# Kernel tuning notes

Hardware: AMD Instinct MI355X
Metric: run time of the kernel (lower is better)

The kernel has to match this reference:

```python
import jax, jax.numpy as jnp
import numpy as np

B, N, D = 128, 512, 128      # graphs, nodes/graph, feature dim
KEEP_RATIO = 0.5
K = int(KEEP_RATIO * N)      # kept nodes per graph (fixed -> jit friendly)
EDGE_P = 0.05                # random graph edge density


def setup_inputs() -> dict:
    key = jax.random.key(0)
    k1, k2, k3 = jax.random.split(key, 3)
    # random symmetric binary adjacency without self loops, per graph block
    u = jax.random.uniform(k1, (B, N, N))
    a0 = (u < EDGE_P).astype(jnp.float32)
    a0 = jnp.maximum(a0, jnp.swapaxes(a0, 1, 2))
    eye = jnp.eye(N, dtype=jnp.float32)
    a0 = a0 * (1.0 - eye)
    # normalized input adjacency: D^-0.5 (A0 + I) D^-0.5 (as `normalization` does)
    a_hat = a0 + eye
    dinv = a_hat.sum(-1) ** -0.5
    adjacency = a_hat * dinv[:, :, None] * dinv[:, None, :]   # [B,N,N]
    input_feature = jax.random.normal(k2, (B, N, D), dtype=jnp.float32)
    graph_indicator = jnp.repeat(jnp.arange(B, dtype=jnp.int32), N)  # [B*N]
    # attn_gcn params: Linear(D -> 1) kaiming-style init, zero bias
    weight = jax.random.normal(k3, (D, 1), dtype=jnp.float32) * (2.0 / D) ** 0.5
    bias = jnp.zeros((1,), dtype=jnp.float32)
    return {"adjacency": adjacency, "input_feature": input_feature,
            "graph_indicator": graph_indicator, "weight": weight, "bias": bias}


def reference(adjacency, input_feature, graph_indicator, weight, bias):
    # --- attention GCN: Z = A @ (X W) + b, then tanh ---
    support = jnp.einsum('bnd,do->bno', input_feature, weight)      # [B,N,1]
    score = jnp.einsum('bnm,bmo->bno', adjacency, support) + bias   # [B,N,1]
    attn = jnp.tanh(score[..., 0])                                  # [B,N]
    # --- top_rank: per-graph top-K by score; mask preserves node order ---
    _, idx = jax.lax.top_k(attn, K)                                 # [B,K]
    idx = jnp.sort(idx, axis=-1)                                    # original node order
    # --- hidden = X[mask] * attn[mask] ---
    kept_x = jnp.take_along_axis(input_feature, idx[:, :, None], axis=1)  # [B,K,D]
    kept_s = jnp.take_along_axis(attn, idx, axis=1)                       # [B,K]
    hidden = (kept_x * kept_s[:, :, None]).reshape(B * K, D)
    mask_graph_indicator = jnp.repeat(jnp.arange(B, dtype=graph_indicator.dtype), K)
    # --- filter_adjacency: binarize off-diagonal structure, gather, renormalize ---
    eye_n = jnp.eye(N, dtype=adjacency.dtype)
    a_bin = jnp.where((adjacency != 0) & (eye_n == 0), 1.0, 0.0)    # [B,N,N]
    rows = jnp.take_along_axis(a_bin, idx[:, :, None], axis=1)      # [B,K,N]
    sub = jnp.take_along_axis(rows, idx[:, None, :], axis=2)        # [B,K,K]
    a_hat = sub + jnp.eye(K, dtype=adjacency.dtype)
    dinv = a_hat.sum(-1) ** -0.5
    mask_adjacency = a_hat * dinv[:, :, None] * dinv[:, None, :]    # [B,K,K]
    return hidden, mask_graph_indicator, mask_adjacency
```

## Files before the change

kernel.cpp:

```cpp
#include <hip/hip_runtime.h>
#include <hip/hip_bf16.h>
#include <math.h>

#define BGR 128
#define NND 512
#define DFD 128
#define KKP 256

typedef unsigned int uint;
typedef unsigned long long ull;

__global__ __launch_bounds__(256) void k_support(const float* __restrict__ X,
                                                 const float* __restrict__ W,
                                                 float* __restrict__ sup) {
    __shared__ float w_s[DFD];
    int t = threadIdx.x;
    if (t < DFD) w_s[t] = W[t];
    __syncthreads();
    int node = blockIdx.x * 64 + (t >> 2);
    int q = t & 3;
    const float4* xp = (const float4*)(X + (size_t)node * DFD + q * 32);
    const float4* wp = (const float4*)(w_s + q * 32);
    float sum = 0.f;
#pragma unroll
    for (int i = 0; i < 8; ++i) {
        float4 x = xp[i], w = wp[i];
        sum += x.x * w.x + x.y * w.y + x.z * w.z + x.w * w.w;
    }
    sum += __shfl_xor(sum, 1);
    sum += __shfl_xor(sum, 2);
    if (q == 0) sup[node] = sum;
}

__global__ __launch_bounds__(256) void k_score(const float* __restrict__ A,
                                               const float* __restrict__ sup,
                                               const float* __restrict__ bias,
                                               float* __restrict__ attn,
                                               ull* __restrict__ bm) {
    __shared__ float sup_s[NND];
    int b = blockIdx.x >> 6;
    int rblk = blockIdx.x & 63;
    int t = threadIdx.x;
    sup_s[t] = sup[b * NND + t];
    sup_s[256 + t] = sup[b * NND + 256 + t];
    __syncthreads();
    int wave = t >> 6, l = t & 63;
    float bias0 = bias[0];
    const float4* sp = (const float4*)sup_s;
    float4 s0 = sp[l], s1 = sp[64 + l];
#pragma unroll
    for (int r = 0; r < 2; ++r) {
        int row = rblk * 8 + wave * 2 + r;
        const float4* ap = (const float4*)(A + ((size_t)b * NND + row) * NND);
        float4 a0 = ap[l], a1 = ap[64 + l];
        float sum = a0.x * s0.x + a0.y * s0.y + a0.z * s0.z + a0.w * s0.w
                  + a1.x * s1.x + a1.y * s1.y + a1.z * s1.z + a1.w * s1.w;
        int c0 = 4 * l;
        ull m[8];
        m[0] = __ballot(a0.x != 0.f && (c0 + 0) != row);
        m[1] = __ballot(a0.y != 0.f && (c0 + 1) != row);
        m[2] = __ballot(a0.z != 0.f && (c0 + 2) != row);
        m[3] = __ballot(a0.w != 0.f && (c0 + 3) != row);
        m[4] = __ballot(a1.x != 0.f && (256 + c0 + 0) != row);
        m[5] = __ballot(a1.y != 0.f && (256 + c0 + 1) != row);
        m[6] = __ballot(a1.z != 0.f && (256 + c0 + 2) != row);
        m[7] = __ballot(a1.w != 0.f && (256 + c0 + 3) != row);
#pragma unroll
        for (int off = 32; off >= 1; off >>= 1) sum += __shfl_down(sum, off);
        if (l == 0) {
            attn[b * NND + row] = tanhf(sum + bias0);
            ull* bp = bm + ((size_t)b * NND + row) * 8;
#pragma unroll
            for (int k = 0; k < 8; ++k) bp[k] = m[k];
        }
    }
}

__global__ __launch_bounds__(512) void k_fuse(const float* __restrict__ X,
                                              const float* __restrict__ attn,
                                              const uint* __restrict__ bm,
                                              float* __restrict__ out_hidden,
                                              float* __restrict__ out_gi,
                                              uint* __restrict__ bits,
                                              float* __restrict__ dinv) {
    __shared__ float attn_s[NND];
    __shared__ uint km[16];
    __shared__ int idx_s[KKP];
    __shared__ uint4 bm_s4[KKP][4];
    __shared__ uint bits_s[KKP][8];
    int b = blockIdx.x, t = threadIdx.x;
    attn_s[t] = attn[b * NND + t];
    __syncthreads();
    int wave = t >> 6, l = t & 63;

    float a = attn_s[t];
    int r = 0;
    const float4* ap4 = (const float4*)attn_s;
    for (int jj = 0; jj < 128; ++jj) {
        float4 v = ap4[jj];
        int j0 = jj * 4;
        r += (v.x > a || (v.x == a && j0     < t)) ? 1 : 0;
        r += (v.y > a || (v.y == a && j0 + 1 < t)) ? 1 : 0;
        r += (v.z > a || (v.z == a && j0 + 2 < t)) ? 1 : 0;
        r += (v.w > a || (v.w == a && j0 + 3 < t)) ? 1 : 0;
    }
    bool keep = r < KKP;
    ull mk = __ballot(keep);
    if (l == 0) { km[wave * 2] = (uint)mk; km[wave * 2 + 1] = (uint)(mk >> 32); }
    __syncthreads();
    if (keep) {
        int w = t >> 5, pos = 0;
        for (int u = 0; u < w; ++u) pos += __popc(km[u]);
        pos += __popc(km[w] & ((1u << (t & 31)) - 1u));
        idx_s[pos] = t;
    }
    if (t < KKP) out_gi[b * KKP + t] = (float)b;
    __syncthreads();

    {
        int i = t >> 1, half = t & 1;
        const uint4* src = (const uint4*)(bm + ((size_t)b * NND + idx_s[i]) * 16) + half * 2;
        bm_s4[i][half * 2]     = src[0];
        bm_s4[i][half * 2 + 1] = src[1];
    }
    __syncthreads();

    const uint* bmw = (const uint*)bm_s4;
    int j = t & 255;
    int jn = idx_s[j];
    int widx = ((jn >> 8) * 4 + (jn & 3)) * 2 + ((jn >> 7) & 1);
    int bitpos = (jn >> 2) & 31;
    int rowoff = t >> 8;
    int wq = (t >> 6) & 3;
    for (int ii = 0; ii < KKP; ii += 2) {
        int row = ii + rowoff;
        uint kb = (bmw[row * 16 + widx] >> bitpos) & 1u;
        ull mb = __ballot(kb != 0u);
        if (l == 0) {
            bits_s[row][wq * 2]     = (uint)mb;
            bits_s[row][wq * 2 + 1] = (uint)(mb >> 32);
            uint* gp = bits + ((size_t)b * KKP + row) * 8 + wq * 2;
            gp[0] = (uint)mb;
            gp[1] = (uint)(mb >> 32);
        }
    }
    __syncthreads();
    if (t < KKP) {
        int s = 1;
#pragma unroll
        for (int k = 0; k < 8; ++k) s += __popc(bits_s[t][k]);
        dinv[b * KKP + t] = 1.0f / sqrtf((float)s);
    }

    for (int r2 = 0; r2 < 32; ++r2) {
        int k = wave * 32 + r2;
        int node = idx_s[k];
        float s = attn_s[node];
        const float2* xp = (const float2*)(X + ((size_t)b * NND + node) * DFD);
        float2 v = xp[l];
        v.x *= s; v.y *= s;
        ((float2*)(out_hidden + ((size_t)b * KKP + k) * DFD))[l] = v;
    }
}

__global__ __launch_bounds__(256) void k_norm(const uint* __restrict__ bits,
                                              const float* __restrict__ dinv,
                                              float* __restrict__ out_adj) {
    __shared__ float dinv_s[KKP];
    int b = blockIdx.x >> 5;
    int rblk = blockIdx.x & 31;
    int t = threadIdx.x, wave = t >> 6, l = t & 63;
    dinv_s[t] = dinv[b * KKP + t];
    __syncthreads();
    float4 dj = ((const float4*)dinv_s)[l];
    const float* djp = &dj.x;
#pragma unroll
    for (int r = 0; r < 2; ++r) {
        int i = rblk * 8 + wave * 2 + r;
        float di = dinv_s[i];
        const uint* bp = bits + ((size_t)b * KKP + i) * 8;
        uint word = bp[l >> 3];
        int j0 = l * 4;
        float4 v;
        float* pv = &v.x;
#pragma unroll
        for (int c = 0; c < 4; ++c) {
            int j = j0 + c;
            float ah = ((word >> (j & 31)) & 1u) ? 1.0f : 0.0f;
            if (j == i) ah += 1.0f;
            pv[c] = ah * di * djp[c];
        }
        ((float4*)(out_adj + ((size_t)b * KKP + i) * KKP))[l] = v;
    }
}

extern "C" void kernel_launch(void* const* d_in, const int* in_sizes, int n_in,
                              void* d_out, int out_size, void* d_ws, size_t ws_size,
                              hipStream_t stream) {
    const float* A    = (const float*)d_in[0];
    const float* X    = (const float*)d_in[1];
    const float* W    = (const float*)d_in[3];
    const float* bias = (const float*)d_in[4];

    float* out        = (float*)d_out;
    float* out_hidden = out;
    float* out_gi     = out + (size_t)BGR * KKP * DFD;
    float* out_adj    = out_gi + (size_t)BGR * KKP;

    float* sup  = (float*)d_ws;
    float* attn = sup + (size_t)BGR * NND;
    ull*   bm   = (ull*)(attn + (size_t)BGR * NND);
    uint*  bits = (uint*)(bm + (size_t)BGR * NND * 8);
    float* dinv = (float*)(bits + (size_t)BGR * KKP * 8);

    k_support<<<BGR * NND / 64, 256, 0, stream>>>(X, W, sup);
    k_score<<<BGR * 64, 256, 0, stream>>>(A, sup, bias, attn, bm);
    k_fuse<<<BGR, 512, 0, stream>>>(X, attn, (const uint*)bm, out_hidden, out_gi, bits, dinv);
    k_norm<<<BGR * 32, 256, 0, stream>>>(bits, dinv, out_adj);
}
```

Baseline: 71.01 us.

## Move hidden-feature gather out of per-graph kernel into wide tail kernel

The gather-and-scale of kept node features was done by only 128 blocks inside the per-graph selection kernel. It now runs in a new tail kernel with thousands of blocks, which also takes over the adjacency normalization work in fewer, larger blocks. The selection kernel writes the kept indices to a workspace buffer. The goal is to spread the 16MB hidden copy across the whole GPU instead of 128 blocks, at the cost of an extra global index write and read.

```diff
diff --git a/kernel.cpp b/kernel.cpp
--- a/kernel.cpp
+++ b/kernel.cpp
@@ -6,6 +6,7 @@
 #define NND 512
 #define DFD 128
 #define KKP 256
+#define HIDBLK 4096
 
 typedef unsigned int uint;
 typedef unsigned long long ull;
@@ -76,11 +77,10 @@
     }
 }
 
-__global__ __launch_bounds__(512) void k_fuse(const float* __restrict__ X,
-                                              const float* __restrict__ attn,
+__global__ __launch_bounds__(512) void k_fuse(const float* __restrict__ attn,
                                               const uint* __restrict__ bm,
-                                              float* __restrict__ out_hidden,
                                               float* __restrict__ out_gi,
+                                              int* __restrict__ gidx,
                                               uint* __restrict__ bits,
                                               float* __restrict__ dinv) {
     __shared__ float attn_s[NND];
@@ -113,6 +113,7 @@
         for (int u = 0; u < w; ++u) pos += __popc(km[u]);
         pos += __popc(km[w] & ((1u << (t & 31)) - 1u));
         idx_s[pos] = t;
+        gidx[b * KKP + pos] = t;
     }
     if (t < KKP) out_gi[b * KKP + t] = (float)b;
     __syncthreads();
@@ -151,46 +152,55 @@
         for (int k = 0; k < 8; ++k) s += __popc(bits_s[t][k]);
         dinv[b * KKP + t] = 1.0f / sqrtf((float)s);
     }
-
-    for (int r2 = 0; r2 < 32; ++r2) {
-        int k = wave * 32 + r2;
-        int node = idx_s[k];
-        float s = attn_s[node];
-        const float2* xp = (const float2*)(X + ((size_t)b * NND + node) * DFD);
-        float2 v = xp[l];
-        v.x *= s; v.y *= s;
-        ((float2*)(out_hidden + ((size_t)b * KKP + k) * DFD))[l] = v;
-    }
-}
-
-__global__ __launch_bounds__(256) void k_norm(const uint* __restrict__ bits,
+}
+
+__global__ __launch_bounds__(256) void k_tail(const float* __restrict__ X,
+                                              const float* __restrict__ attn,
+                                              const int* __restrict__ gidx,
+                                              const uint* __restrict__ bits,
                                               const float* __restrict__ dinv,
+                                              float* __restrict__ out_hidden,
                                               float* __restrict__ out_adj) {
     __shared__ float dinv_s[KKP];
-    int b = blockIdx.x >> 5;
-    int rblk = blockIdx.x & 31;
+    int blk = blockIdx.x;
     int t = threadIdx.x, wave = t >> 6, l = t & 63;
-    dinv_s[t] = dinv[b * KKP + t];
-    __syncthreads();
-    float4 dj = ((const float4*)dinv_s)[l];
-    const float* djp = &dj.x;
-#pragma unroll
-    for (int r = 0; r < 2; ++r) {
-        int i = rblk * 8 + wave * 2 + r;
-        float di = dinv_s[i];
-        const uint* bp = bits + ((size_t)b * KKP + i) * 8;
-        uint word = bp[l >> 3];
-        int j0 = l * 4;
-        float4 v;
-        float* pv = &v.x;
-#pragma unroll
-        for (int c = 0; c < 4; ++c) {
-            int j = j0 + c;
-            float ah = ((word >> (j & 31)) & 1u) ? 1.0f : 0.0f;
-            if (j == i) ah += 1.0f;
-            pv[c] = ah * di * djp[c];
-        }
-        ((float4*)(out_adj + ((size_t)b * KKP + i) * KKP))[l] = v;
+    if (blk < HIDBLK) {
+        int r0 = blk * 8 + wave * 2;
+#pragma unroll
+        for (int rr = 0; rr < 2; ++rr) {
+            int r = r0 + rr;
+            int b = r >> 8;
+            int node = gidx[r];
+            float s = attn[b * NND + node];
+            const float2* xp = (const float2*)(X + ((size_t)b * NND + node) * DFD);
+            float2 v = xp[l];
+            v.x *= s; v.y *= s;
+            ((float2*)(out_hidden + (size_t)r * DFD))[l] = v;
+        }
+    } else {
+        int nb = blk - HIDBLK;
+        int b = nb >> 2, q = nb & 3;
+        if (t < KKP) dinv_s[t] = dinv[b * KKP + t];
+        __syncthreads();
+        float4 dj = ((const float4*)dinv_s)[l];
+        const float* djp = &dj.x;
+        for (int rr = 0; rr < 16; ++rr) {
+            int i = q * 64 + wave * 16 + rr;
+            float di = dinv_s[i];
+            const uint* bp = bits + ((size_t)b * KKP + i) * 8;
+            uint word = bp[l >> 3];
+            int j0 = l * 4;
+            float4 v;
+            float* pv = &v.x;
+#pragma unroll
+            for (int c = 0; c < 4; ++c) {
+                int j = j0 + c;
+                float ah = ((word >> (j & 31)) & 1u) ? 1.0f : 0.0f;
+                if (j == i) ah += 1.0f;
+                pv[c] = ah * di * djp[c];
+            }
+            ((float4*)(out_adj + ((size_t)b * KKP + i) * KKP))[l] = v;
+        }
     }
 }
 
@@ -212,9 +222,11 @@
     ull*   bm   = (ull*)(attn + (size_t)BGR * NND);
     uint*  bits = (uint*)(bm + (size_t)BGR * NND * 8);
     float* dinv = (float*)(bits + (size_t)BGR * KKP * 8);
+    int*   gidx = (int*)(dinv + (size_t)BGR * KKP);
 
     k_support<<<BGR * NND / 64, 256, 0, stream>>>(X, W, sup);
     k_score<<<BGR * 64, 256, 0, stream>>>(A, sup, bias, attn, bm);
-    k_fuse<<<BGR, 512, 0, stream>>>(X, attn, (const uint*)bm, out_hidden, out_gi, bits, dinv);
-    k_norm<<<BGR * 32, 256, 0, stream>>>(bits, dinv, out_adj);
-}
+    k_fuse<<<BGR, 512, 0, stream>>>(attn, (const uint*)bm, out_gi, gidx, bits, dinv);
+    k_tail<<<HIDBLK + BGR * 4, 256, 0, stream>>>(X, attn, gidx, bits, dinv,
+                                                 out_hidden, out_adj);
+}
```

Measured after the change: 70.53 us. About the same (-0.7%).

## Fuse top-k selection and adjacency normalization into one per-graph-quarter kernel

Applied to the files above, without the earlier changes.

Merges the selection kernel and the normalized-adjacency kernel into a single kernel launched with four blocks per graph. Each block recomputes the ranking and the sub-adjacency bitmask in shared memory, then writes only its quarter of the hidden rows and adjacency rows. This removes one launch and the global-memory round trip for the intermediate bits and dinv buffers, and spreads the work over four times as many blocks. In exchange, the rank computation and bitmask extraction are done four times per graph.

```diff
diff --git a/kernel.cpp b/kernel.cpp
--- a/kernel.cpp
+++ b/kernel.cpp
@@ -76,22 +76,22 @@
     }
 }
 
-__global__ __launch_bounds__(512) void k_fuse(const float* __restrict__ X,
+__global__ __launch_bounds__(512) void k_mega(const float* __restrict__ X,
                                               const float* __restrict__ attn,
                                               const uint* __restrict__ bm,
                                               float* __restrict__ out_hidden,
                                               float* __restrict__ out_gi,
-                                              uint* __restrict__ bits,
-                                              float* __restrict__ dinv) {
+                                              float* __restrict__ out_adj) {
     __shared__ float attn_s[NND];
     __shared__ uint km[16];
     __shared__ int idx_s[KKP];
     __shared__ uint4 bm_s4[KKP][4];
     __shared__ uint bits_s[KKP][8];
-    int b = blockIdx.x, t = threadIdx.x;
+    __shared__ float dinv_s[KKP];
+    int b = blockIdx.x >> 2, q = blockIdx.x & 3;
+    int t = threadIdx.x, wave = t >> 6, l = t & 63;
     attn_s[t] = attn[b * NND + t];
     __syncthreads();
-    int wave = t >> 6, l = t & 63;
 
     float a = attn_s[t];
     int r = 0;
@@ -114,7 +114,6 @@
         pos += __popc(km[w] & ((1u << (t & 31)) - 1u));
         idx_s[pos] = t;
     }
-    if (t < KKP) out_gi[b * KKP + t] = (float)b;
     __syncthreads();
 
     {
@@ -123,11 +122,22 @@
         bm_s4[i][half * 2]     = src[0];
         bm_s4[i][half * 2 + 1] = src[1];
     }
+
+    if (t < KKP) out_gi[b * KKP + t] = (float)b;
+#pragma unroll
+    for (int it = 0; it < 8; ++it) {
+        int k = q * 64 + it * 8 + wave;
+        int node = idx_s[k];
+        float s = attn_s[node];
+        const float2* xp = (const float2*)(X + ((size_t)b * NND + node) * DFD);
+        float2 v = xp[l];
+        v.x *= s; v.y *= s;
+        ((float2*)(out_hidden + ((size_t)b * KKP + k) * DFD))[l] = v;
+    }
     __syncthreads();
 
     const uint* bmw = (const uint*)bm_s4;
-    int j = t & 255;
-    int jn = idx_s[j];
+    int jn = idx_s[t & 255];
     int widx = ((jn >> 8) * 4 + (jn & 3)) * 2 + ((jn >> 7) & 1);
     int bitpos = (jn >> 2) & 31;
     int rowoff = t >> 8;
@@ -139,9 +149,6 @@
         if (l == 0) {
             bits_s[row][wq * 2]     = (uint)mb;
             bits_s[row][wq * 2 + 1] = (uint)(mb >> 32);
-            uint* gp = bits + ((size_t)b * KKP + row) * 8 + wq * 2;
-            gp[0] = (uint)mb;
-            gp[1] = (uint)(mb >> 32);
         }
     }
     __syncthreads();
@@ -149,37 +156,17 @@
         int s = 1;
 #pragma unroll
         for (int k = 0; k < 8; ++k) s += __popc(bits_s[t][k]);
-        dinv[b * KKP + t] = 1.0f / sqrtf((float)s);
-    }
-
-    for (int r2 = 0; r2 < 32; ++r2) {
-        int k = wave * 32 + r2;
-        int node = idx_s[k];
-        float s = attn_s[node];
-        const float2* xp = (const float2*)(X + ((size_t)b * NND + node) * DFD);
-        float2 v = xp[l];
-        v.x *= s; v.y *= s;
-        ((float2*)(out_hidden + ((size_t)b * KKP + k) * DFD))[l] = v;
-    }
-}
-
-__global__ __launch_bounds__(256) void k_norm(const uint* __restrict__ bits,
-                                              const float* __restrict__ dinv,
-                                              float* __restrict__ out_adj) {
-    __shared__ float dinv_s[KKP];
-    int b = blockIdx.x >> 5;
-    int rblk = blockIdx.x & 31;
-    int t = threadIdx.x, wave = t >> 6, l = t & 63;
-    dinv_s[t] = dinv[b * KKP + t];
-    __syncthreads();
+        dinv_s[t] = 1.0f / sqrtf((float)s);
+    }
+    __syncthreads();
+
     float4 dj = ((const float4*)dinv_s)[l];
     const float* djp = &dj.x;
 #pragma unroll
-    for (int r = 0; r < 2; ++r) {
-        int i = rblk * 8 + wave * 2 + r;
+    for (int it = 0; it < 8; ++it) {
+        int i = q * 64 + it * 8 + wave;
         float di = dinv_s[i];
-        const uint* bp = bits + ((size_t)b * KKP + i) * 8;
-        uint word = bp[l >> 3];
+        uint word = bits_s[i][l >> 3];
         int j0 = l * 4;
         float4 v;
         float* pv = &v.x;
@@ -210,11 +197,9 @@
     float* sup  = (float*)d_ws;
     float* attn = sup + (size_t)BGR * NND;
     ull*   bm   = (ull*)(attn + (size_t)BGR * NND);
-    uint*  bits = (uint*)(bm + (size_t)BGR * NND * 8);
-    float* dinv = (float*)(bits + (size_t)BGR * KKP * 8);
 
     k_support<<<BGR * NND / 64, 256, 0, stream>>>(X, W, sup);
     k_score<<<BGR * 64, 256, 0, stream>>>(A, sup, bias, attn, bm);
-    k_fuse<<<BGR, 512, 0, stream>>>(X, attn, (const uint*)bm, out_hidden, out_gi, bits, dinv);
-    k_norm<<<BGR * 32, 256, 0, stream>>>(bits, dinv, out_adj);
-}
+    k_mega<<<BGR * 4, 512, 0, stream>>>(X, attn, (const uint*)bm,
+                                        out_hidden, out_gi, out_adj);
+}
```

Result: no change. 70.32 us (-1.0%).
